# Optimization experiments

Hardware: AMD Instinct MI355X
Metric: run time of the kernel (lower is better)

The kernel has to match this reference:

```python
import jax, jax.numpy as jnp
import numpy as np

IN_DIM, OUT_DIM = 1024, 1024
GRID_SIZE, K = 8, 3
TOKENS = 8192


def b_splines(x, grid, k):
    # x: [B, in_dim], grid: [in_dim, grid_size + 2k + 1]
    x = x[..., None]  # [B, in_dim, 1]
    # order-0 indicator bases: [B, in_dim, grid_size + 2k]
    bases = ((x >= grid[:, :-1]) & (x < grid[:, 1:])).astype(x.dtype)
    # Cox-de Boor recursion up to order k -> [B, in_dim, grid_size + k]
    for kk in range(1, k + 1):
        left = (x - grid[:, : -(kk + 1)]) / (grid[:, kk:-1] - grid[:, : -(kk + 1)])
        right = (grid[:, kk + 1:] - x) / (grid[:, kk + 1:] - grid[:, 1:-kk])
        bases = left * bases[..., :-1] + right * bases[..., 1:]
    return bases


def setup_inputs() -> dict:
    key = jax.random.key(0)
    k1, k2, k3 = jax.random.split(key, 3)
    x = jax.random.normal(k1, (TOKENS, IN_DIM), dtype=jnp.float32)
    # grid buffer: arange(-k, grid_size+k+1) * step + grid_range[0], repeated per in_dim
    grid_range = (-1.0, 1.0)
    step = (grid_range[1] - grid_range[0]) / GRID_SIZE
    grid_row = np.arange(-K, GRID_SIZE + K + 1, dtype=np.float32) * step + grid_range[0]
    grid = jnp.asarray(np.tile(grid_row, (IN_DIM, 1)))  # [in_dim, 15]
    coeff = jax.random.normal(k2, (OUT_DIM, IN_DIM, GRID_SIZE + K), dtype=jnp.float32) * 0.1
    scale_base = 1.0 / np.sqrt(IN_DIM) + jax.random.normal(k3, (OUT_DIM, IN_DIM), dtype=jnp.float32) * 0.1
    scale_spline = jnp.ones((1,), dtype=jnp.float32)
    return {"x": x, "grid": grid, "coeff": coeff, "scale_base": scale_base,
            "scale_spline": scale_spline}


def reference(x, grid, coeff, scale_base, scale_spline):
    splines = b_splines(x, grid, K)                      # [B, in, G+K]
    y_b = jnp.matmul(jax.nn.silu(x), scale_base.T)       # [B, out]
    w = coeff * scale_spline                             # scalar broadcast [out, in, G+K]
    y_spline = jnp.einsum('big,oig->bo', splines, w)     # [B, out]
    return y_b + y_spline
```

## Files before the change

### kernel.cpp

```cpp
#include <hip/hip_runtime.h>
#include <hip/hip_bf16.h>
#include <stdint.h>

typedef __attribute__((ext_vector_type(8))) short short8;
typedef __attribute__((ext_vector_type(16))) float floatx16;
typedef unsigned short u16;

#define IN_DIM  1024
#define OUT_DIM 1024
#define NG      11
#define GK      12
#define KDIM    (IN_DIM * GK)
#define TOKENS  8192
#define MT      64
#define BK      96
#define PB      104
#define NOPS    26
#define GBK     64
#define GR      9
#define GOPS    18

__device__ __forceinline__ u16 f2bf(float f) {
  uint32_t u = __float_as_uint(f);
  uint32_t r = (u + 0x7fffu + ((u >> 16) & 1u)) >> 16;
  return (u16)r;
}

__global__ __launch_bounds__(256) void pack_wt_kernel(
    const float* __restrict__ coeff, const float* __restrict__ sb,
    const float* __restrict__ ss_p, u16* __restrict__ Wt)
{
  __shared__ float cf[256 * NG];
  __shared__ __align__(16) u16 st[256 * GK];
  const int tid = threadIdx.x;
  const int b   = blockIdx.x;
  const int o   = b >> 2;
  const int i0  = (b & 3) * 256;
  const float* cbase = coeff + (size_t)o * (IN_DIM * NG) + (size_t)i0 * NG;
#pragma unroll
  for (int p = 0; p < NG; ++p) cf[p * 256 + tid] = cbase[p * 256 + tid];
  const float ss  = ss_p[0];
  const float sbv = sb[(size_t)o * IN_DIM + i0 + tid];
  __syncthreads();
  const float* cp = cf + tid * NG;
  u16 h[GK];
#pragma unroll
  for (int g = 0; g < NG; ++g) h[g] = f2bf(cp[g] * ss);
  h[NG] = f2bf(sbv);
  uint64_t V0 = (uint64_t)h[0] | ((uint64_t)h[1] << 16) | ((uint64_t)h[2] << 32) | ((uint64_t)h[3] << 48);
  uint64_t V1 = (uint64_t)h[4] | ((uint64_t)h[5] << 16) | ((uint64_t)h[6] << 32) | ((uint64_t)h[7] << 48);
  uint64_t V2 = (uint64_t)h[8] | ((uint64_t)h[9] << 16) | ((uint64_t)h[10] << 32) | ((uint64_t)h[11] << 48);
  uint64_t* sp = (uint64_t*)(st + tid * GK);
  sp[0] = V0; sp[1] = V1; sp[2] = V2;
  __syncthreads();
  const uint4* src = (const uint4*)st;
  uint4* dst = (uint4*)(Wt + (size_t)b * (256 * GK));
  dst[tid] = src[tid];
  if (tid < 128) dst[256 + tid] = src[256 + tid];
}

__device__ __forceinline__ void expand_regs(float x, float g0, float inv_h,
                                            uint64_t& V0, uint64_t& V1, uint64_t& V2)
{
  float t  = (x - g0) * inv_h;
  float fc = floorf(t);
  int   c  = (int)fc;
  float u  = t - fc;
  float u2 = u * u;
  float w1 = 1.0f - u;
  float b0 = (w1 * w1 * w1) * (1.0f / 6.0f);
  float b1 = (0.5f * u - 1.0f) * u2 + (2.0f / 3.0f);
  float b2 = ((-0.5f * u + 0.5f) * u + 0.5f) * u + (1.0f / 6.0f);
  float b3 = (u2 * u) * (1.0f / 6.0f);
  float sil = x / (1.0f + __expf(-x));

  uint64_t P = (uint64_t)f2bf(b0) | ((uint64_t)f2bf(b1) << 16)
             | ((uint64_t)f2bf(b2) << 32) | ((uint64_t)f2bf(b3) << 48);
  int  k  = c - 3;
  bool cv = (c >= 0) && (c <= 13);
  int  kneg = (k < 0) ? -k : 0;
  uint64_t Pc = cv ? (P >> (16 * kneg)) : 0ull;
  uint32_t sh = (uint32_t)(16 * ((k < 0) ? 0 : k));

  V0 = (sh < 64)  ? (Pc << (sh & 63)) : 0ull;
  V1 = (sh == 0)  ? 0ull :
       (sh < 64)  ? (Pc >> ((64 - sh) & 63)) :
       (sh < 128) ? (Pc << ((sh - 64) & 63)) : 0ull;
  V2 = (sh <= 64) ? 0ull :
       (sh < 128) ? (Pc >> ((128 - sh) & 63)) :
                    (Pc << ((sh - 128) & 63));
  V2 = (V2 & 0x0000FFFFFFFFFFFFull) | ((uint64_t)f2bf(sil) << 48);
}

__device__ __forceinline__ void async16(const u16* g, u16* l) {
  __builtin_amdgcn_global_load_lds(
      (const __attribute__((address_space(1))) uint32_t*)g,
      (__attribute__((address_space(3))) uint32_t*)l,
      16, 0, 0);
}

__global__ __launch_bounds__(256) void expand_x_kernel(
    const float* __restrict__ X, const float* __restrict__ grid,
    u16* __restrict__ Aexp)
{
  __shared__ __align__(16) uint4 st[1536];
  const int tid = threadIdx.x;
  const int row = blockIdx.x;
  const float g0    = grid[0];
  const float inv_h = 1.0f / (grid[1] - grid[0]);

  float4 xv = *(const float4*)(X + (size_t)row * IN_DIM + tid * 4);
  uint64_t ev[12];
  expand_regs(xv.x, g0, inv_h, ev[0], ev[1], ev[2]);
  expand_regs(xv.y, g0, inv_h, ev[3], ev[4], ev[5]);
  expand_regs(xv.z, g0, inv_h, ev[6], ev[7], ev[8]);
  expand_regs(xv.w, g0, inv_h, ev[9], ev[10], ev[11]);
#pragma unroll
  for (int j = 0; j < 6; ++j) {
    uint4 w;
    w.x = (uint32_t)ev[2*j];     w.y = (uint32_t)(ev[2*j] >> 32);
    w.z = (uint32_t)ev[2*j+1];   w.w = (uint32_t)(ev[2*j+1] >> 32);
    st[tid * 6 + j] = w;
  }
  __syncthreads();
  uint4* dst = (uint4*)(Aexp + (size_t)row * KDIM);
#pragma unroll
  for (int j = 0; j < 6; ++j) dst[j * 256 + tid] = st[j * 256 + tid];
}

__global__ __launch_bounds__(256, 4) void gemm_pre_kernel(
    const u16* __restrict__ A, const u16* __restrict__ Wt,
    float* __restrict__ out, float* __restrict__ part, int k_iters)
{
  __shared__ __align__(16) u16 As[128 * GR * 8];
  __shared__ __align__(16) u16 Bs[128 * GR * 8];

  const int tid  = threadIdx.x;
  const int lane = tid & 63;
  const int wave = tid >> 6;
  const int s    = blockIdx.x >> 9;
  const int r    = blockIdx.x & 511;
  const int bm   = r & 63;
  const int bn   = r >> 6;
  const int wm   = (wave >> 1) * 64;
  const int wn   = (wave & 1) * 64;
  const int l31  = lane & 31;
  const int g8   = lane >> 5;

  floatx16 acc[2][2];
#pragma unroll
  for (int a = 0; a < 2; ++a)
#pragma unroll
    for (int b = 0; b < 2; ++b)
#pragma unroll
      for (int rr = 0; rr < 16; ++rr) acc[a][b][rr] = 0.f;

  const size_t k0 = (size_t)s * k_iters * GBK;
  const u16* asrc[5]; const u16* bsrc[5]; int doff[5]; bool act[5];
#pragma unroll
  for (int j = 0; j < 5; ++j) {
    int o  = wave + 4 * j;
    act[j] = (o < GOPS);
    int oc = act[j] ? o : (GOPS - 1);
    int gidx  = oc * 64 + lane;
    int row   = gidx / 9;
    int chunk = gidx - row * 9;
    int c8    = (chunk == 8) ? 0 : chunk;
    asrc[j] = A  + (size_t)(bm * 128 + row) * KDIM + k0 + c8 * 8;
    bsrc[j] = Wt + (size_t)(bn * 128 + row) * KDIM + k0 + c8 * 8;
    doff[j] = oc * 512;
  }

  for (int it = 0; it < k_iters; ++it) {
    __syncthreads();
#pragma unroll
    for (int j = 0; j < 5; ++j)
      if (act[j]) async16(asrc[j] + (size_t)it * GBK, As + doff[j]);
#pragma unroll
    for (int j = 0; j < 5; ++j)
      if (act[j]) async16(bsrc[j] + (size_t)it * GBK, Bs + doff[j]);
    __syncthreads();

#pragma unroll
    for (int t = 0; t < 4; ++t) {
      short8 af[2], bf[2];
#pragma unroll
      for (int ss2 = 0; ss2 < 2; ++ss2) {
        af[ss2] = *(const short8*)&As[(wm + ss2 * 32 + l31) * (GR * 8) + (2 * t + g8) * 8];
        bf[ss2] = *(const short8*)&Bs[(wn + ss2 * 32 + l31) * (GR * 8) + (2 * t + g8) * 8];
      }
#pragma unroll
      for (int sm = 0; sm < 2; ++sm)
#pragma unroll
        for (int sn = 0; sn < 2; ++sn)
          acc[sm][sn] = __builtin_amdgcn_mfma_f32_32x32x16_bf16(af[sm], bf[sn], acc[sm][sn], 0, 0, 0);
    }
  }

  float* op = (s == 0) ? out : part;
#pragma unroll
  for (int sm = 0; sm < 2; ++sm)
#pragma unroll
    for (int sn = 0; sn < 2; ++sn) {
      const int row0 = bm * 128 + wm + sm * 32 + 4 * g8;
      const int col  = bn * 128 + wn + sn * 32 + l31;
#pragma unroll
      for (int reg = 0; reg < 16; ++reg) {
        int row = row0 + (reg & 3) + 8 * (reg >> 2);
        op[(size_t)row * OUT_DIM + col] = acc[sm][sn][reg];
      }
    }
}

__global__ __launch_bounds__(256) void reduce_kernel(
    float* __restrict__ out, const float* __restrict__ part)
{
  size_t i = (size_t)blockIdx.x * 256 + threadIdx.x;
  float4* o = (float4*)out;
  const float4* p = (const float4*)part;
  float4 a = o[i], b = p[i];
  a.x += b.x; a.y += b.y; a.z += b.z; a.w += b.w;
  o[i] = a;
}

__global__ __launch_bounds__(256, 3) void gemm_fused_kernel(
    const float* __restrict__ X, const float* __restrict__ grid,
    const u16* __restrict__ Wt, float* __restrict__ out, float* __restrict__ part,
    int k_iters)
{
  __shared__ __align__(16) u16 As[128 * PB];
  __shared__ __align__(16) u16 Bs[128 * PB];

  const int tid  = threadIdx.x;
  const int lane = tid & 63;
  const int wave = tid >> 6;
  const int mt8  = MT * 8;
  const int s    = blockIdx.x / mt8;
  const int r    = blockIdx.x - s * mt8;
  const int bm   = r % MT;
  const int bn   = r / MT;
  const int wm = (wave >> 1) * 64;
  const int wn = (wave & 1) * 64;

  const float g0    = grid[0];
  const float inv_h = 1.0f / (grid[1] - grid[0]);

  floatx16 acc[2][2];
#pragma unroll
  for (int a = 0; a < 2; ++a)
#pragma unroll
    for (int b = 0; b < 2; ++b)
#pragma unroll
      for (int rr = 0; rr < 16; ++rr) acc[a][b][rr] = 0.f;

  const int kb_u16 = s * k_iters * BK;
  const u16* bsrc[7];
  u16*       bdst[7];
  bool       bact[7];
#pragma unroll
  for (int j = 0; j < 7; ++j) {
    int o  = wave + 4 * j;
    bact[j] = (o < NOPS);
    int oc = bact[j] ? o : (NOPS - 1);
    int gidx  = oc * 64 + lane;
    int row   = gidx / 13;
    int chunk = gidx - row * 13;
    int c8    = (chunk == 12) ? 0 : chunk;
    bsrc[j] = Wt + (size_t)(bn * 128 + row) * KDIM + kb_u16 + c8 * 8;
    bdst[j] = Bs + oc * 512;
  }

  const int arow = tid & 127;
  const int half = tid >> 7;
  const float* xp = X + (size_t)(bm * 128 + arow) * IN_DIM + s * (k_iters * 8) + half * 4;
  uint4* awp = (uint4*)(As + arow * PB + half * 48);

  const int l31 = lane & 31;
  const int g   = lane >> 5;

  float4 xv = *(const float4*)xp;

  for (int it = 0; it < k_iters; ++it) {
    uint64_t ev[12];
    expand_regs(xv.x, g0, inv_h, ev[0], ev[1], ev[2]);
    expand_regs(xv.y, g0, inv_h, ev[3], ev[4], ev[5]);
    expand_regs(xv.z, g0, inv_h, ev[6], ev[7], ev[8]);
    expand_regs(xv.w, g0, inv_h, ev[9], ev[10], ev[11]);
    if (it + 1 < k_iters) xv = *(const float4*)(xp + (size_t)(it + 1) * 8);

    __syncthreads();

#pragma unroll
    for (int j = 0; j < 7; ++j)
      if (bact[j]) async16(bsrc[j] + (size_t)it * BK, bdst[j]);

#pragma unroll
    for (int j = 0; j < 6; ++j) {
      uint4 w;
      w.x = (uint32_t)ev[2*j];     w.y = (uint32_t)(ev[2*j] >> 32);
      w.z = (uint32_t)ev[2*j+1];   w.w = (uint32_t)(ev[2*j+1] >> 32);
      awp[j] = w;
    }

    __syncthreads();

#pragma unroll
    for (int t = 0; t < 6; ++t) {
      const int cc = 2 * t + g;
      short8 af[2], bf[2];
#pragma unroll
      for (int ss2 = 0; ss2 < 2; ++ss2) {
        af[ss2] = *(const short8*)&As[(wm + ss2 * 32 + l31) * PB + cc * 8];
        bf[ss2] = *(const short8*)&Bs[(wn + ss2 * 32 + l31) * PB + cc * 8];
      }
#pragma unroll
      for (int sm = 0; sm < 2; ++sm)
#pragma unroll
        for (int sn = 0; sn < 2; ++sn)
          acc[sm][sn] = __builtin_amdgcn_mfma_f32_32x32x16_bf16(af[sm], bf[sn], acc[sm][sn], 0, 0, 0);
    }
  }
  __syncthreads();

  float* op = (s == 0) ? out : part;
#pragma unroll
  for (int sm = 0; sm < 2; ++sm)
#pragma unroll
    for (int sn = 0; sn < 2; ++sn) {
      const int row0 = bm * 128 + wm + sm * 32 + 4 * g;
      const int col  = bn * 128 + wn + sn * 32 + l31;
#pragma unroll
      for (int reg = 0; reg < 16; ++reg) {
        int row = row0 + (reg & 3) + 8 * (reg >> 2);
        op[(size_t)row * OUT_DIM + col] = acc[sm][sn][reg];
      }
    }
}

extern "C" void kernel_launch(void* const* d_in, const int* in_sizes, int n_in,
                              void* d_out, int out_size, void* d_ws, size_t ws_size,
                              hipStream_t stream) {
  const float* x     = (const float*)d_in[0];
  const float* grid  = (const float*)d_in[1];
  const float* coeff = (const float*)d_in[2];
  const float* sb    = (const float*)d_in[3];
  const float* ss    = (const float*)d_in[4];
  float* out = (float*)d_out;

  u16* Wt = (u16*)d_ws;
  const size_t wt_bytes   = (size_t)OUT_DIM * KDIM * 2;
  const size_t aexp_bytes = (size_t)TOKENS * KDIM * 2;
  const size_t part_bytes = (size_t)TOKENS * OUT_DIM * 4;

  pack_wt_kernel<<<(OUT_DIM * IN_DIM) / 256, 256, 0, stream>>>(coeff, sb, ss, Wt);

  if (ws_size >= wt_bytes + aexp_bytes + part_bytes) {
    u16*   Aexp = (u16*)((char*)d_ws + wt_bytes);
    float* part = (float*)((char*)d_ws + wt_bytes + aexp_bytes);
    expand_x_kernel<<<TOKENS, 256, 0, stream>>>(x, grid, Aexp);
    gemm_pre_kernel<<<512 * 2, 256, 0, stream>>>(Aexp, Wt, out, part, 96);
    reduce_kernel<<<(TOKENS * OUT_DIM / 4) / 256, 256, 0, stream>>>(out, part);
  } else if (ws_size >= wt_bytes + aexp_bytes) {
    u16* Aexp = (u16*)((char*)d_ws + wt_bytes);
    expand_x_kernel<<<TOKENS, 256, 0, stream>>>(x, grid, Aexp);
    gemm_pre_kernel<<<512, 256, 0, stream>>>(Aexp, Wt, out, nullptr, 192);
  } else if (ws_size >= wt_bytes + part_bytes) {
    float* part = (float*)((char*)d_ws + wt_bytes);
    gemm_fused_kernel<<<MT * 8 * 2, 256, 0, stream>>>(x, grid, Wt, out, part, 64);
    reduce_kernel<<<(TOKENS * OUT_DIM / 4) / 256, 256, 0, stream>>>(out, part);
  } else {
    gemm_fused_kernel<<<MT * 8, 256, 0, stream>>>(x, grid, Wt, out, nullptr, 128);
  }
}
```

Baseline: 422.4 us.

## Enlarge GEMM tiles to 256x256 with double-buffered async LDS loads

The precomputed-A GEMM moves from 128x128 tiles with 4 waves to 256x256 tiles with 8 waves, each wave computing a 128x64 sub-tile. Global-to-LDS loads are double-buffered with explicit vmcnt waits so the next K-slice loads while the current one is multiplied, and s_setprio raises MFMA priority. The expand kernel now processes 4 rows per block. The aim is more data reuse per LDS byte and hidden load latency, at the cost of more LDS and registers, fewer blocks (256 with split-K), and possible wave-quantization or occupancy loss.

After: 423.2 us. About the same (+0.2%).

```diff
diff --git a/kernel.cpp b/kernel.cpp
--- a/kernel.cpp
+++ b/kernel.cpp
@@ -17,8 +17,9 @@
 #define PB      104
 #define NOPS    26
 #define GBK     64
-#define GR      9
-#define GOPS    18
+#define G2R     9
+#define G2OPS   36
+#define ABUF    (256 * 72)
 
 __device__ __forceinline__ u16 f2bf(float f) {
   uint32_t u = __float_as_uint(f);
@@ -105,51 +106,54 @@
 {
   __shared__ __align__(16) uint4 st[1536];
   const int tid = threadIdx.x;
-  const int row = blockIdx.x;
   const float g0    = grid[0];
   const float inv_h = 1.0f / (grid[1] - grid[0]);
 
-  float4 xv = *(const float4*)(X + (size_t)row * IN_DIM + tid * 4);
-  uint64_t ev[12];
-  expand_regs(xv.x, g0, inv_h, ev[0], ev[1], ev[2]);
-  expand_regs(xv.y, g0, inv_h, ev[3], ev[4], ev[5]);
-  expand_regs(xv.z, g0, inv_h, ev[6], ev[7], ev[8]);
-  expand_regs(xv.w, g0, inv_h, ev[9], ev[10], ev[11]);
-#pragma unroll
-  for (int j = 0; j < 6; ++j) {
-    uint4 w;
-    w.x = (uint32_t)ev[2*j];     w.y = (uint32_t)(ev[2*j] >> 32);
-    w.z = (uint32_t)ev[2*j+1];   w.w = (uint32_t)(ev[2*j+1] >> 32);
-    st[tid * 6 + j] = w;
-  }
-  __syncthreads();
-  uint4* dst = (uint4*)(Aexp + (size_t)row * KDIM);
-#pragma unroll
-  for (int j = 0; j < 6; ++j) dst[j * 256 + tid] = st[j * 256 + tid];
-}
-
-__global__ __launch_bounds__(256, 4) void gemm_pre_kernel(
+  for (int rr = 0; rr < 4; ++rr) {
+    const int row = blockIdx.x * 4 + rr;
+    float4 xv = *(const float4*)(X + (size_t)row * IN_DIM + tid * 4);
+    uint64_t ev[12];
+    expand_regs(xv.x, g0, inv_h, ev[0], ev[1], ev[2]);
+    expand_regs(xv.y, g0, inv_h, ev[3], ev[4], ev[5]);
+    expand_regs(xv.z, g0, inv_h, ev[6], ev[7], ev[8]);
+    expand_regs(xv.w, g0, inv_h, ev[9], ev[10], ev[11]);
+    if (rr) __syncthreads();
+#pragma unroll
+    for (int j = 0; j < 6; ++j) {
+      uint4 w;
+      w.x = (uint32_t)ev[2*j];     w.y = (uint32_t)(ev[2*j] >> 32);
+      w.z = (uint32_t)ev[2*j+1];   w.w = (uint32_t)(ev[2*j+1] >> 32);
+      st[tid * 6 + j] = w;
+    }
+    __syncthreads();
+    uint4* dst = (uint4*)(Aexp + (size_t)row * KDIM);
+#pragma unroll
+    for (int j = 0; j < 6; ++j) dst[j * 256 + tid] = st[j * 256 + tid];
+  }
+}
+
+__global__ __launch_bounds__(512, 2) void gemm_pre_kernel(
     const u16* __restrict__ A, const u16* __restrict__ Wt,
     float* __restrict__ out, float* __restrict__ part, int k_iters)
 {
-  __shared__ __align__(16) u16 As[128 * GR * 8];
-  __shared__ __align__(16) u16 Bs[128 * GR * 8];
+  __shared__ __align__(16) u16 As[2 * ABUF];
+  __shared__ __align__(16) u16 Bs[2 * ABUF];
 
   const int tid  = threadIdx.x;
   const int lane = tid & 63;
   const int wave = tid >> 6;
-  const int s    = blockIdx.x >> 9;
-  const int r    = blockIdx.x & 511;
-  const int bm   = r & 63;
-  const int bn   = r >> 6;
-  const int wm   = (wave >> 1) * 64;
-  const int wn   = (wave & 1) * 64;
+  const int s    = blockIdx.x >> 7;
+  const int r    = blockIdx.x & 127;
+  const int bm   = r & 31;
+  const int bn   = r >> 5;
+  const int wm   = (wave >> 2) * 128;
+  const int wn   = (wave & 3) * 64;
   const int l31  = lane & 31;
   const int g8   = lane >> 5;
 
-  floatx16 acc[2][2];
-#pragma unroll
-  for (int a = 0; a < 2; ++a)
+  floatx16 acc[4][2];
+#pragma unroll
+  for (int a = 0; a < 4; ++a)
 #pragma unroll
     for (int b = 0; b < 2; ++b)
 #pragma unroll
@@ -159,55 +163,79 @@
   const u16* asrc[5]; const u16* bsrc[5]; int doff[5]; bool act[5];
 #pragma unroll
   for (int j = 0; j < 5; ++j) {
-    int o  = wave + 4 * j;
-    act[j] = (o < GOPS);
-    int oc = act[j] ? o : (GOPS - 1);
+    int o  = wave + 8 * j;
+    act[j] = (o < G2OPS);
+    int oc = act[j] ? o : (G2OPS - 1);
     int gidx  = oc * 64 + lane;
     int row   = gidx / 9;
     int chunk = gidx - row * 9;
     int c8    = (chunk == 8) ? 0 : chunk;
-    asrc[j] = A  + (size_t)(bm * 128 + row) * KDIM + k0 + c8 * 8;
-    bsrc[j] = Wt + (size_t)(bn * 128 + row) * KDIM + k0 + c8 * 8;
+    asrc[j] = A  + (size_t)(bm * 256 + row) * KDIM + k0 + c8 * 8;
+    bsrc[j] = Wt + (size_t)(bn * 256 + row) * KDIM + k0 + c8 * 8;
     doff[j] = oc * 512;
   }
 
-  for (int it = 0; it < k_iters; ++it) {
-    __syncthreads();
-#pragma unroll
-    for (int j = 0; j < 5; ++j)
-      if (act[j]) async16(asrc[j] + (size_t)it * GBK, As + doff[j]);
-#pragma unroll
-    for (int j = 0; j < 5; ++j)
-      if (act[j]) async16(bsrc[j] + (size_t)it * GBK, Bs + doff[j]);
-    __syncthreads();
-
-#pragma unroll
-    for (int t = 0; t < 4; ++t) {
-      short8 af[2], bf[2];
-#pragma unroll
-      for (int ss2 = 0; ss2 < 2; ++ss2) {
-        af[ss2] = *(const short8*)&As[(wm + ss2 * 32 + l31) * (GR * 8) + (2 * t + g8) * 8];
-        bf[ss2] = *(const short8*)&Bs[(wn + ss2 * 32 + l31) * (GR * 8) + (2 * t + g8) * 8];
+  const int NT = k_iters;
+
+#pragma unroll
+  for (int j = 0; j < 5; ++j) if (act[j]) async16(asrc[j], As + doff[j]);
+#pragma unroll
+  for (int j = 0; j < 5; ++j) if (act[j]) async16(bsrc[j], Bs + doff[j]);
+  asm volatile("s_waitcnt vmcnt(0)" ::: "memory");
+  __builtin_amdgcn_s_barrier();
+  __builtin_amdgcn_sched_barrier(0);
+#pragma unroll
+  for (int j = 0; j < 5; ++j) if (act[j]) async16(asrc[j] + GBK, As + ABUF + doff[j]);
+#pragma unroll
+  for (int j = 0; j < 5; ++j) if (act[j]) async16(bsrc[j] + GBK, Bs + ABUF + doff[j]);
+
+  for (int t = 0; t < NT; ++t) {
+    const u16* Ab = As + (t & 1) * ABUF;
+    const u16* Bb = Bs + (t & 1) * ABUF;
+
+    __builtin_amdgcn_s_setprio(1);
+#pragma unroll
+    for (int ks = 0; ks < 4; ++ks) {
+      short8 bf0 = *(const short8*)&Bb[(wn +      l31) * 72 + (2 * ks + g8) * 8];
+      short8 bf1 = *(const short8*)&Bb[(wn + 32 + l31) * 72 + (2 * ks + g8) * 8];
+#pragma unroll
+      for (int m = 0; m < 4; ++m) {
+        short8 af = *(const short8*)&Ab[(wm + m * 32 + l31) * 72 + (2 * ks + g8) * 8];
+        acc[m][0] = __builtin_amdgcn_mfma_f32_32x32x16_bf16(af, bf0, acc[m][0], 0, 0, 0);
+        acc[m][1] = __builtin_amdgcn_mfma_f32_32x32x16_bf16(af, bf1, acc[m][1], 0, 0, 0);
       }
-#pragma unroll
-      for (int sm = 0; sm < 2; ++sm)
-#pragma unroll
-        for (int sn = 0; sn < 2; ++sn)
-          acc[sm][sn] = __builtin_amdgcn_mfma_f32_32x32x16_bf16(af[sm], bf[sn], acc[sm][sn], 0, 0, 0);
-    }
+    }
+    __builtin_amdgcn_s_setprio(0);
+
+    __builtin_amdgcn_s_barrier();
+    __builtin_amdgcn_sched_barrier(0);
+    if (t + 2 < NT) {
+      u16* Ad = As + (t & 1) * ABUF;
+      u16* Bd = Bs + (t & 1) * ABUF;
+      const size_t ko = (size_t)(t + 2) * GBK;
+#pragma unroll
+      for (int j = 0; j < 5; ++j) if (act[j]) async16(asrc[j] + ko, Ad + doff[j]);
+#pragma unroll
+      for (int j = 0; j < 5; ++j) if (act[j]) async16(bsrc[j] + ko, Bd + doff[j]);
+      asm volatile("s_waitcnt vmcnt(8)" ::: "memory");
+    } else {
+      asm volatile("s_waitcnt vmcnt(0)" ::: "memory");
+    }
+    __builtin_amdgcn_s_barrier();
+    __builtin_amdgcn_sched_barrier(0);
   }
 
   float* op = (s == 0) ? out : part;
 #pragma unroll
-  for (int sm = 0; sm < 2; ++sm)
-#pragma unroll
-    for (int sn = 0; sn < 2; ++sn) {
-      const int row0 = bm * 128 + wm + sm * 32 + 4 * g8;
-      const int col  = bn * 128 + wn + sn * 32 + l31;
+  for (int m = 0; m < 4; ++m)
+#pragma unroll
+    for (int n = 0; n < 2; ++n) {
+      const int row0 = bm * 256 + wm + m * 32 + 4 * g8;
+      const int col  = bn * 256 + wn + n * 32 + l31;
 #pragma unroll
       for (int reg = 0; reg < 16; ++reg) {
         int row = row0 + (reg & 3) + 8 * (reg >> 2);
-        op[(size_t)row * OUT_DIM + col] = acc[sm][sn][reg];
+        op[(size_t)row * OUT_DIM + col] = acc[m][n][reg];
       }
     }
 }
@@ -357,13 +385,13 @@
   if (ws_size >= wt_bytes + aexp_bytes + part_bytes) {
     u16*   Aexp = (u16*)((char*)d_ws + wt_bytes);
     float* part = (float*)((char*)d_ws + wt_bytes + aexp_bytes);
-    expand_x_kernel<<<TOKENS, 256, 0, stream>>>(x, grid, Aexp);
-    gemm_pre_kernel<<<512 * 2, 256, 0, stream>>>(Aexp, Wt, out, part, 96);
+    expand_x_kernel<<<TOKENS / 4, 256, 0, stream>>>(x, grid, Aexp);
+    gemm_pre_kernel<<<128 * 2, 512, 0, stream>>>(Aexp, Wt, out, part, 96);
     reduce_kernel<<<(TOKENS * OUT_DIM / 4) / 256, 256, 0, stream>>>(out, part);
   } else if (ws_size >= wt_bytes + aexp_bytes) {
     u16* Aexp = (u16*)((char*)d_ws + wt_bytes);
-    expand_x_kernel<<<TOKENS, 256, 0, stream>>>(x, grid, Aexp);
-    gemm_pre_kernel<<<512, 256, 0, stream>>>(Aexp, Wt, out, nullptr, 192);
+    expand_x_kernel<<<TOKENS / 4, 256, 0, stream>>>(x, grid, Aexp);
+    gemm_pre_kernel<<<128, 512, 0, stream>>>(Aexp, Wt, out, nullptr, 192);
   } else if (ws_size >= wt_bytes + part_bytes) {
     float* part = (float*)((char*)d_ws + wt_bytes);
     gemm_fused_kernel<<<MT * 8 * 2, 256, 0, stream>>>(x, grid, Wt, out, part, 64);
```
